# Performance work log

Measured on AMD Instinct MI355X. Metric: run time of the kernel, lower is better.

The kernel has to match this reference:

```python
import jax, jax.numpy as jnp
import numpy as np

B, S, D, H = 2, 2048, 1024, 16
DH = D // H
EPS = 1e-6
MASK_VALUE = -1e30


def layer_norm(x, g, b):
    mu = jnp.mean(x, axis=-1, keepdims=True)
    var = jnp.mean(jnp.square(x - mu), axis=-1, keepdims=True)
    return (x - mu) * jax.lax.rsqrt(var + EPS) * g + b


def setup_inputs() -> dict:
    key = jax.random.key(0)
    ks = jax.random.split(key, 8)
    scale = 1.0 / np.sqrt(D)
    return {
        "x": jax.random.normal(ks[0], (B, S, D), dtype=jnp.float32),
        "mask": jnp.ones((B, S), dtype=jnp.float32),
        "Wq": jax.random.normal(ks[1], (D, D), dtype=jnp.float32) * scale,
        "bq": jnp.zeros((D,), dtype=jnp.float32),
        "Wk": jax.random.normal(ks[2], (D, D), dtype=jnp.float32) * scale,
        "bk": jnp.zeros((D,), dtype=jnp.float32),
        "Wv": jax.random.normal(ks[3], (D, D), dtype=jnp.float32) * scale,
        "bv": jnp.zeros((D,), dtype=jnp.float32),
        "Wo": jax.random.normal(ks[4], (D, D), dtype=jnp.float32) * scale,
        "bo": jnp.zeros((D,), dtype=jnp.float32),
        "g1": jnp.ones((D,), dtype=jnp.float32),
        "b1": jnp.zeros((D,), dtype=jnp.float32),
        "g2": jnp.ones((D,), dtype=jnp.float32),
        "b2": jnp.zeros((D,), dtype=jnp.float32),
    }


def reference(x, mask, Wq, bq, Wk, bk, Wv, bv, Wo, bo, g1, b1, g2, b2):
    # Dropout is identity in eval mode.
    h = layer_norm(x, g1, b1)  # [B,S,D]
    # Conv1D with kernel_size=1 == per-token linear with weight [out,in]
    def proj(W, bias):
        return (jnp.einsum('bsd,ed->bse', h, W) + bias).reshape(B, S, H, DH).transpose(0, 2, 1, 3)
    q = proj(Wq, bq)  # [B,H,S,DH]
    k = proj(Wk, bk)
    v = proj(Wv, bv)
    scores = jnp.einsum('bhqd,bhkd->bhqk', q, k) / np.sqrt(DH)
    scores = scores + (1.0 - mask)[:, None, None, :] * MASK_VALUE
    probs = jax.nn.softmax(scores, axis=-1)
    attn = jnp.einsum('bhqk,bhkd->bhqd', probs, v)  # [B,H,S,DH]
    attn = attn.transpose(0, 2, 1, 3).reshape(B, S, D)
    residual = attn + x
    out = layer_norm(residual, g2, b2)
    out = jnp.einsum('bsd,ed->bse', out, Wo) + bo
    return out + residual
```

## Files before the change

kernel.cpp:

```cpp
#include <hip/hip_runtime.h>
#include <hip/hip_bf16.h>

typedef unsigned short u16;
typedef unsigned int u32;
typedef __attribute__((ext_vector_type(8))) short s16x8;
typedef __attribute__((ext_vector_type(4))) float f32x4;
typedef __attribute__((ext_vector_type(16))) float f32x16;
typedef __attribute__((ext_vector_type(4))) u16 u16x4;

#define SLEN 2048
#define DMODEL 1024
#define NHEAD 16
#define DHEAD 64
#define LDQK 2048
#define VSTRIDE 4096
#define LOG2E 1.4426950408889634f

__device__ __forceinline__ u16 f2bf(float f) {
  union { __hip_bfloat16 h; u16 u; } c;
  c.h = __float2bfloat16(f);
  return c.u;
}

__device__ __forceinline__ u32 pk2(float a, float b) {
  union { __hip_bfloat162 h2; u32 u; } c;
  float2 f2; f2.x = a; f2.y = b;
  c.h2 = __float22bfloat162_rn(f2);
  return c.u;
}

__device__ __forceinline__ void gload_lds16(const u16* gsrc, u16* lds) {
  __builtin_amdgcn_global_load_lds((const __attribute__((address_space(1))) void*)gsrc,
                                   (__attribute__((address_space(3))) void*)lds, 16, 0, 0);
}

__device__ __forceinline__ s16x8 make_pa(int hi, const float* p) {
  u32 A0 = pk2(p[0], p[1]), A1 = pk2(p[2], p[3]);
  u32 A2 = pk2(p[4], p[5]), A3 = pk2(p[6], p[7]);
  u32 S0 = (u32)__shfl_xor((int)A0, 32);
  u32 S1 = (u32)__shfl_xor((int)A1, 32);
  u32 S2 = (u32)__shfl_xor((int)A2, 32);
  u32 S3 = (u32)__shfl_xor((int)A3, 32);
  union { u32 w[4]; s16x8 v; } pw;
  pw.w[0] = hi ? S2 : A0;
  pw.w[1] = hi ? S3 : A1;
  pw.w[2] = hi ? A2 : S0;
  pw.w[3] = hi ? A3 : S1;
  return pw.v;
}

__device__ __forceinline__ void ln_body(
    int row, int t, const float* __restrict__ xa,
    const float* __restrict__ g, const float* __restrict__ bb,
    u16* __restrict__ outb) {
  const size_t base = (size_t)row * DMODEL;
  float4 v = *((const float4*)(xa + base) + t);
  float s1 = v.x + v.y + v.z + v.w;
  float s2 = v.x * v.x + v.y * v.y + v.z * v.z + v.w * v.w;
#pragma unroll
  for (int d = 1; d < 64; d <<= 1) { s1 += __shfl_xor(s1, d); s2 += __shfl_xor(s2, d); }
  __shared__ float red[8];
  if ((t & 63) == 0) { red[(t >> 6) * 2] = s1; red[(t >> 6) * 2 + 1] = s2; }
  __syncthreads();
  s1 = red[0] + red[2] + red[4] + red[6];
  s2 = red[1] + red[3] + red[5] + red[7];
  const float mu = s1 * (1.0f / 1024.0f);
  const float var = s2 * (1.0f / 1024.0f) - mu * mu;
  const float rs = rsqrtf(var + 1e-6f);
  const int c = t * 4;
  float o0 = (v.x - mu) * rs * g[c + 0] + bb[c + 0];
  float o1 = (v.y - mu) * rs * g[c + 1] + bb[c + 1];
  float o2 = (v.z - mu) * rs * g[c + 2] + bb[c + 2];
  float o3 = (v.w - mu) * rs * g[c + 3] + bb[c + 3];
  u16x4 o = { f2bf(o0), f2bf(o1), f2bf(o2), f2bf(o3) };
  *((u16x4*)(outb + base) + t) = o;
}

__global__ __launch_bounds__(256) void prep_kernel(
    const float* __restrict__ x,
    const float* __restrict__ Wq, const float* __restrict__ Wk, const float* __restrict__ Wv,
    const float* __restrict__ Wo, const float* __restrict__ bq, const float* __restrict__ bk,
    const float* __restrict__ bv, const float* __restrict__ mask,
    const float* __restrict__ g1, const float* __restrict__ b1,
    u16* __restrict__ Wqkv, u16* __restrict__ Wob, float* __restrict__ bias_qkv,
    float* __restrict__ am, u32* __restrict__ amflag, u16* __restrict__ h_bf) {
  const int bid = blockIdx.x;
  if (bid >= 4096) {
    ln_body(bid - 4096, threadIdx.x, x, g1, b1, h_bf);
    return;
  }
  const int t = bid * 256 + threadIdx.x;
  float4 v;
  u16* dst;
  if (t < 786432) {
    const int idx = t * 4;
    const int sec = idx >> 20;
    const int off = idx & 1048575;
    const float* src = (sec == 0) ? Wq : (sec == 1) ? Wk : Wv;
    v = *(const float4*)(src + off);
    dst = Wqkv + idx;
  } else {
    const int idx = (t - 786432) * 4;
    v = *(const float4*)(Wo + idx);
    dst = Wob + idx;
  }
  u16x4 o = { f2bf(v.x), f2bf(v.y), f2bf(v.z), f2bf(v.w) };
  *(u16x4*)dst = o;
  if (t < 768) {
    const int idx = t * 4;
    const int sec = idx >> 10;
    const int off = idx & 1023;
    const float* src = (sec == 0) ? bq : (sec == 1) ? bk : bv;
    *(float4*)(bias_qkv + idx) = *(const float4*)(src + off);
  }
  if (t < 1024) {
    const int idx = t * 4;
    float4 mk = *(const float4*)(mask + idx);
    const float C = -1e30f * LOG2E;
    float4 o2 = { (1.f - mk.x) * C, (1.f - mk.y) * C,
                  (1.f - mk.z) * C, (1.f - mk.w) * C };
    *(float4*)(am + idx) = o2;
  }
  if (t < 64) {
    const int bb = t >> 5, tile = t & 31;
    u32 fl = 0;
    for (int j = 0; j < 64; ++j)
      fl |= (mask[bb * SLEN + tile * 64 + j] != 1.0f) ? 1u : 0u;
    amflag[t] = fl;
  }
}

__global__ __launch_bounds__(256) void ln_kernel(
    const float* __restrict__ xa, const float* __restrict__ g,
    const float* __restrict__ bb, u16* __restrict__ outb) {
  ln_body(blockIdx.x, threadIdx.x, xa, g, bb, outb);
}

__device__ __forceinline__ void gemm_core(
    const u16* __restrict__ A, const u16* __restrict__ B,
    const float* __restrict__ bias, const float* __restrict__ res,
    u16* __restrict__ outb, float* __restrict__ outf,
    int M, int N, int K, int m0, int n0, int mode,
    u16* As, u16* Bs) {
  const int t = threadIdx.x;
  const int l = t & 63, w = t >> 6, lr = l & 15, lg = l >> 4;
  const int wm = w >> 1, wn = w & 1;

  const f32x4 z4 = {0.f, 0.f, 0.f, 0.f};
  f32x4 acc[4][4];
#pragma unroll
  for (int i = 0; i < 4; ++i)
#pragma unroll
    for (int j = 0; j < 4; ++j) acc[i][j] = z4;

  for (int kt = 0; kt < K; kt += 64) {
#pragma unroll
    for (int p = 0; p < 4; ++p) {
      const int idx = p * 256 + t;
      const int row = idx >> 3;
      const int blk = idx & 7;
      const int sb = blk ^ (row & 7);
      gload_lds16(A + (size_t)(m0 + row) * K + kt + sb * 8, &As[idx * 8]);
      gload_lds16(B + (size_t)(n0 + row) * K + kt + sb * 8, &Bs[idx * 8]);
    }
    asm volatile("s_waitcnt vmcnt(0)" ::: "memory");
    __syncthreads();

#pragma unroll
    for (int ks = 0; ks < 2; ++ks) {
      s16x8 af[4], bfr[4];
#pragma unroll
      for (int mi = 0; mi < 4; ++mi) {
        const int row = wm * 64 + mi * 16 + lr;
        af[mi] = *(const s16x8*)&As[row * 64 + (((ks * 4 + lg) ^ (row & 7)) & 7) * 8];
      }
#pragma unroll
      for (int ni = 0; ni < 4; ++ni) {
        const int row = wn * 64 + ni * 16 + lr;
        bfr[ni] = *(const s16x8*)&Bs[row * 64 + (((ks * 4 + lg) ^ (row & 7)) & 7) * 8];
      }
#pragma unroll
      for (int mi = 0; mi < 4; ++mi)
#pragma unroll
        for (int ni = 0; ni < 4; ++ni)
          acc[mi][ni] = __builtin_amdgcn_mfma_f32_16x16x32_bf16(af[mi], bfr[ni], acc[mi][ni], 0, 0, 0);
    }
    __syncthreads();
  }

#pragma unroll
  for (int mi = 0; mi < 4; ++mi)
#pragma unroll
    for (int ni = 0; ni < 4; ++ni) {
      const int col = n0 + wn * 64 + ni * 16 + lr;
#pragma unroll
      for (int r = 0; r < 4; ++r) {
        const int rowb = m0 + wm * 64 + mi * 16 + lg * 4 + r;
        float vv = acc[mi][ni][r];
        if (mode == 2) {
          vv += bias[rowb];
          outb[(size_t)rowb * N + col] = f2bf(vv);
        } else if (mode == 0) {
          vv += bias[col];
          if (col < 1024) vv *= 0.125f * LOG2E;
          outb[(size_t)rowb * N + col] = f2bf(vv);
        } else {
          vv += bias[col] + res[(size_t)rowb * N + col];
          outf[(size_t)rowb * N + col] = vv;
        }
      }
    }
}

__global__ __launch_bounds__(256) void qkv_gemm_kernel(
    const u16* __restrict__ h_bf, const u16* __restrict__ Wqkv,
    const float* __restrict__ biasq, u16* __restrict__ qkbuf, u16* __restrict__ vT) {
  __shared__ __align__(16) u16 As[128 * 64];
  __shared__ __align__(16) u16 Bs[128 * 64];
  const int bid = blockIdx.x;
  const int lid = (bid & 7) * 96 + (bid >> 3);
  if (lid < 512) {
    gemm_core(h_bf, Wqkv, biasq, nullptr, qkbuf, nullptr,
              4096, 2048, 1024, (lid & 31) * 128, (lid >> 5) * 128, 0, As, Bs);
  } else {
    const int id = lid - 512;
    gemm_core(Wqkv + (size_t)2048 * 1024, h_bf, biasq + 2048, nullptr, vT, nullptr,
              1024, 4096, 1024, (id & 7) * 128, (id >> 3) * 128, 2, As, Bs);
  }
}

__global__ __launch_bounds__(256) void out_gemm_kernel(
    const u16* __restrict__ h2, const u16* __restrict__ Wob,
    const float* __restrict__ bo, const float* __restrict__ res,
    float* __restrict__ outf) {
  __shared__ __align__(16) u16 As[128 * 64];
  __shared__ __align__(16) u16 Bs[128 * 64];
  const int bid = blockIdx.x;
  const int lid = (bid & 7) * 32 + (bid >> 3);
  gemm_core(h2, Wob, bo, res, nullptr, outf,
            4096, 1024, 1024, (lid & 31) * 128, (lid >> 5) * 128, 1, As, Bs);
}

__global__ __launch_bounds__(256) void attn_kernel(
    const u16* __restrict__ qk, const u16* __restrict__ vt,
    const float* __restrict__ am, const u32* __restrict__ amflag,
    const float* __restrict__ x, float* __restrict__ out) {
  const int did = blockIdx.x;
  const int lid = (did & 7) * 64 + (did >> 3);
  const int qb = lid & 15;
  const int h = (lid >> 4) & 15;
  const int b = lid >> 8;

  const int t = threadIdx.x;
  const int l = t & 63, w = t >> 6;
  const int l31 = l & 31;
  const int hi = l >> 5;
  const int hi4 = hi * 4;
  const int sw = l31 & 7;

  __shared__ __align__(16) u16 Ks[2][64 * 64];
  __shared__ __align__(16) u16 Vs[2][64 * 64];
  __shared__ u32 amFlagS[32];
  __shared__ float bcastS[4][32];

  const int q0 = qb * 128 + w * 32;

  const u16* qrow = qk + (size_t)(b * SLEN + q0 + l31) * LDQK + h * DHEAD + hi * 8;
  s16x8 qf[4];
#pragma unroll
  for (int f = 0; f < 4; ++f) qf[f] = *(const s16x8*)(qrow + f * 16);

  if (t < 32) amFlagS[t] = amflag[b * 32 + t];

  const u16* kbase = qk + (size_t)(b * SLEN) * LDQK + DMODEL + h * DHEAD;
  const u16* vtbase = vt + (size_t)(h * DHEAD) * VSTRIDE + b * SLEN;

#define STAGE(kt, buf)                                                              \
  {                                                                                 \
    _Pragma("unroll")                                                               \
    for (int p = 0; p < 2; ++p) {                                                   \
      const int idx = p * 256 + t;                                                  \
      const int row = idx >> 3;                                                     \
      const int blk = idx & 7;                                                      \
      const int sb = blk ^ (row & 7);                                               \
      gload_lds16(kbase + (size_t)((kt) * 64 + row) * LDQK + sb * 8,                \
                  &Ks[buf][idx * 8]);                                               \
    }                                                                               \
    _Pragma("unroll")                                                               \
    for (int p = 0; p < 2; ++p) {                                                   \
      const int idx = p * 256 + t;                                                  \
      const int dh = idx >> 3;                                                      \
      const int blk = idx & 7;                                                      \
      const int sb = blk ^ (dh & 7);                                                \
      gload_lds16(vtbase + (size_t)dh * VSTRIDE + (kt) * 64 + sb * 8,               \
                  &Vs[buf][idx * 8]);                                               \
    }                                                                               \
  }

  f32x16 oA, oB;
#pragma unroll
  for (int r = 0; r < 16; ++r) { oA[r] = 0.f; oB[r] = 0.f; }
  float lsum = 0.f;

  STAGE(0, 0);
  asm volatile("s_waitcnt vmcnt(0)" ::: "memory");
  __syncthreads();

  int cur = 0;
  for (int kt = 0; kt < SLEN / 64; ++kt) {
    if (kt + 1 < SLEN / 64) STAGE(kt + 1, cur ^ 1);

    f32x16 sA, sB;
#pragma unroll
    for (int r = 0; r < 16; ++r) { sA[r] = 0.f; sB[r] = 0.f; }
    __builtin_amdgcn_s_setprio(1);
#pragma unroll
    for (int f = 0; f < 4; ++f) {
      const int c = 2 * f + hi;
      s16x8 kA = *(const s16x8*)&Ks[cur][l31 * 64 + ((c ^ sw) & 7) * 8];
      s16x8 kB = *(const s16x8*)&Ks[cur][(32 + l31) * 64 + ((c ^ sw) & 7) * 8];
      sA = __builtin_amdgcn_mfma_f32_32x32x16_bf16(kA, qf[f], sA, 0, 0, 0);
      sB = __builtin_amdgcn_mfma_f32_32x32x16_bf16(kB, qf[f], sB, 0, 0, 0);
    }
    __builtin_amdgcn_s_setprio(0);

    const int kv0 = kt * 64;
    if (amFlagS[kt]) {
#pragma unroll
      for (int r = 0; r < 16; ++r) {
        const int rid = (r & 3) + ((r >> 2) << 3) + hi4;
        sA[r] += am[b * SLEN + kv0 + rid];
        sB[r] += am[b * SLEN + kv0 + 32 + rid];
      }
    }

    float pA_[16], pB_[16];
#pragma unroll
    for (int r = 0; r < 16; ++r) {
      pA_[r] = __builtin_amdgcn_exp2f(sA[r]);
      pB_[r] = __builtin_amdgcn_exp2f(sB[r]);
    }
    float s8[8];
#pragma unroll
    for (int i = 0; i < 8; ++i)
      s8[i] = (pA_[2 * i] + pA_[2 * i + 1]) + (pB_[2 * i] + pB_[2 * i + 1]);
#pragma unroll
    for (int i = 0; i < 4; ++i) s8[i] += s8[i + 4];
    s8[0] += s8[2]; s8[1] += s8[3];
    lsum += s8[0] + s8[1];

    s16x8 pa0 = make_pa(hi, pA_);
    s16x8 pa1 = make_pa(hi, pA_ + 8);
    s16x8 pa2 = make_pa(hi, pB_);
    s16x8 pa3 = make_pa(hi, pB_ + 8);

    __builtin_amdgcn_s_setprio(1);
#pragma unroll
    for (int s = 0; s < 4; ++s) {
      const int c = 2 * s + hi;
      s16x8 vA = *(const s16x8*)&Vs[cur][l31 * 64 + ((c ^ sw) & 7) * 8];
      s16x8 vB = *(const s16x8*)&Vs[cur][(32 + l31) * 64 + ((c ^ sw) & 7) * 8];
      const s16x8 pas = (s == 0) ? pa0 : (s == 1) ? pa1 : (s == 2) ? pa2 : pa3;
      oA = __builtin_amdgcn_mfma_f32_32x32x16_bf16(pas, vA, oA, 0, 0, 0);
      oB = __builtin_amdgcn_mfma_f32_32x32x16_bf16(pas, vB, oB, 0, 0, 0);
    }
    __builtin_amdgcn_s_setprio(0);

    asm volatile("s_waitcnt vmcnt(0)" ::: "memory");
    __syncthreads();
    cur ^= 1;
  }

  lsum += __shfl_xor(lsum, 32);
  bcastS[w][l31] = 1.0f / lsum;
  const size_t rowoff = (size_t)(b * SLEN + q0) * DMODEL + h * DHEAD + l31;
  float* outp = out + rowoff;
  const float* xp = x + rowoff;
#pragma unroll
  for (int r = 0; r < 16; ++r) {
    const int rid = (r & 3) + ((r >> 2) << 3) + hi4;
    const float rv = bcastS[w][rid];
    outp[(size_t)rid * DMODEL] = oA[r] * rv + xp[(size_t)rid * DMODEL];
    outp[(size_t)rid * DMODEL + 32] = oB[r] * rv + xp[(size_t)rid * DMODEL + 32];
  }
#undef STAGE
}

extern "C" void kernel_launch(void* const* d_in, const int* in_sizes, int n_in,
                              void* d_out, int out_size, void* d_ws, size_t ws_size,
                              hipStream_t stream) {
  const float* x    = (const float*)d_in[0];
  const float* mask = (const float*)d_in[1];
  const float* Wq   = (const float*)d_in[2];
  const float* bq   = (const float*)d_in[3];
  const float* Wk   = (const float*)d_in[4];
  const float* bk   = (const float*)d_in[5];
  const float* Wv   = (const float*)d_in[6];
  const float* bv   = (const float*)d_in[7];
  const float* Wo   = (const float*)d_in[8];
  const float* bo   = (const float*)d_in[9];
  const float* g1   = (const float*)d_in[10];
  const float* b1   = (const float*)d_in[11];
  const float* g2   = (const float*)d_in[12];
  const float* b2   = (const float*)d_in[13];
  float* out = (float*)d_out;
  char* ws = (char*)d_ws;

  u16*   h_bf  = (u16*)(ws + 0);
  u16*   Wqkv  = (u16*)(ws + ((size_t)8 << 20));
  u16*   Wob   = (u16*)(ws + ((size_t)14 << 20));
  float* biasq = (float*)(ws + ((size_t)16 << 20));
  float* amv   = (float*)(ws + ((size_t)16 << 20) + (64 << 10));
  u32*   amfl  = (u32*)(ws + ((size_t)16 << 20) + (128 << 10));
  u16*   qkbuf = (u16*)(ws + ((size_t)17 << 20));
  u16*   vT2   = (u16*)(ws + ((size_t)33 << 20));
  float* resb  = (float*)(ws + ((size_t)41 << 20));
  u16*   h2_bf = (u16*)(ws + 0);

  prep_kernel<<<8192, 256, 0, stream>>>(x, Wq, Wk, Wv, Wo, bq, bk, bv, mask, g1, b1,
                                        Wqkv, Wob, biasq, amv, amfl, h_bf);
  qkv_gemm_kernel<<<768, 256, 0, stream>>>(h_bf, Wqkv, biasq, qkbuf, vT2);
  attn_kernel<<<512, 256, 0, stream>>>(qkbuf, vT2, amv, amfl, x, resb);
  ln_kernel<<<4096, 256, 0, stream>>>(resb, g2, b2, h2_bf);
  out_gemm_kernel<<<256, 256, 0, stream>>>(h2_bf, Wob, bo, resb, out);
}
```

Baseline: 146.2 us.

## Pipeline GEMM K-loop with four-stage LDS ring and use permlane32 swap in attention

The shared GEMM core moves from a single-buffered 64-wide K tile with a full wait and two barriers per step to a four-buffer ring of 32-wide K tiles. Three tiles are prefetched ahead, with partial vmcnt waits and one barrier per step, so global-to-LDS loads overlap MFMA work. In attention, the P-fragment repack replaces four cross-half shuffles and selects with two v_permlane32_swap instructions. LDS per GEMM block doubles to 64 KB, which may reduce occupancy.

```diff
diff --git a/kernel.cpp b/kernel.cpp
--- a/kernel.cpp
+++ b/kernel.cpp
@@ -34,18 +34,13 @@
                                    (__attribute__((address_space(3))) void*)lds, 16, 0, 0);
 }
 
-__device__ __forceinline__ s16x8 make_pa(int hi, const float* p) {
+__device__ __forceinline__ s16x8 make_pa(const float* p) {
   u32 A0 = pk2(p[0], p[1]), A1 = pk2(p[2], p[3]);
   u32 A2 = pk2(p[4], p[5]), A3 = pk2(p[6], p[7]);
-  u32 S0 = (u32)__shfl_xor((int)A0, 32);
-  u32 S1 = (u32)__shfl_xor((int)A1, 32);
-  u32 S2 = (u32)__shfl_xor((int)A2, 32);
-  u32 S3 = (u32)__shfl_xor((int)A3, 32);
+  asm("v_permlane32_swap_b32 %0, %1" : "+v"(A0), "+v"(A2));
+  asm("v_permlane32_swap_b32 %0, %1" : "+v"(A1), "+v"(A3));
   union { u32 w[4]; s16x8 v; } pw;
-  pw.w[0] = hi ? S2 : A0;
-  pw.w[1] = hi ? S3 : A1;
-  pw.w[2] = hi ? A2 : S0;
-  pw.w[3] = hi ? A3 : S1;
+  pw.w[0] = A0; pw.w[1] = A1; pw.w[2] = A2; pw.w[3] = A3;
   return pw.v;
 }
 
@@ -153,39 +148,61 @@
 #pragma unroll
     for (int j = 0; j < 4; ++j) acc[i][j] = z4;
 
-  for (int kt = 0; kt < K; kt += 64) {
-#pragma unroll
-    for (int p = 0; p < 4; ++p) {
-      const int idx = p * 256 + t;
-      const int row = idx >> 3;
-      const int blk = idx & 7;
-      const int sb = blk ^ (row & 7);
-      gload_lds16(A + (size_t)(m0 + row) * K + kt + sb * 8, &As[idx * 8]);
-      gload_lds16(B + (size_t)(n0 + row) * K + kt + sb * 8, &Bs[idx * 8]);
-    }
-    asm volatile("s_waitcnt vmcnt(0)" ::: "memory");
-    __syncthreads();
-
-#pragma unroll
-    for (int ks = 0; ks < 2; ++ks) {
-      s16x8 af[4], bfr[4];
-#pragma unroll
-      for (int mi = 0; mi < 4; ++mi) {
-        const int row = wm * 64 + mi * 16 + lr;
-        af[mi] = *(const s16x8*)&As[row * 64 + (((ks * 4 + lg) ^ (row & 7)) & 7) * 8];
-      }
-#pragma unroll
-      for (int ni = 0; ni < 4; ++ni) {
-        const int row = wn * 64 + ni * 16 + lr;
-        bfr[ni] = *(const s16x8*)&Bs[row * 64 + (((ks * 4 + lg) ^ (row & 7)) & 7) * 8];
-      }
-#pragma unroll
-      for (int mi = 0; mi < 4; ++mi)
-#pragma unroll
-        for (int ni = 0; ni < 4; ++ni)
-          acc[mi][ni] = __builtin_amdgcn_mfma_f32_16x16x32_bf16(af[mi], bfr[ni], acc[mi][ni], 0, 0, 0);
-    }
-    __syncthreads();
+  const int nt = K >> 5;
+
+#define GSTAGE(tt, buf)                                                         \
+  {                                                                             \
+    _Pragma("unroll")                                                           \
+    for (int p = 0; p < 2; ++p) {                                               \
+      const int c = p * 256 + t;                                                \
+      const int row = c >> 2, blk = c & 3;                                      \
+      const int sb = blk ^ (row & 3);                                           \
+      gload_lds16(A + (size_t)(m0 + row) * K + (tt) * 32 + sb * 8,              \
+                  &As[(buf) * 4096 + c * 8]);                                   \
+    }                                                                           \
+    _Pragma("unroll")                                                           \
+    for (int p = 0; p < 2; ++p) {                                               \
+      const int c = p * 256 + t;                                                \
+      const int row = c >> 2, blk = c & 3;                                      \
+      const int sb = blk ^ (row & 3);                                           \
+      gload_lds16(B + (size_t)(n0 + row) * K + (tt) * 32 + sb * 8,              \
+                  &Bs[(buf) * 4096 + c * 8]);                                   \
+    }                                                                           \
+  }
+
+  GSTAGE(0, 0);
+  GSTAGE(1, 1);
+  GSTAGE(2, 2);
+  asm volatile("s_waitcnt vmcnt(8)" ::: "memory");
+  __builtin_amdgcn_s_barrier();
+
+  for (int tt = 0; tt < nt; ++tt) {
+    const int buf = tt & 3;
+    if (tt + 3 < nt) GSTAGE(tt + 3, (tt + 3) & 3);
+
+    s16x8 af[4], bfr[4];
+#pragma unroll
+    for (int mi = 0; mi < 4; ++mi) {
+      const int row = wm * 64 + mi * 16 + lr;
+      af[mi] = *(const s16x8*)&As[buf * 4096 + row * 32 + ((lg ^ (row & 3)) & 3) * 8];
+    }
+#pragma unroll
+    for (int ni = 0; ni < 4; ++ni) {
+      const int row = wn * 64 + ni * 16 + lr;
+      bfr[ni] = *(const s16x8*)&Bs[buf * 4096 + row * 32 + ((lg ^ (row & 3)) & 3) * 8];
+    }
+    __builtin_amdgcn_s_setprio(1);
+#pragma unroll
+    for (int mi = 0; mi < 4; ++mi)
+#pragma unroll
+      for (int ni = 0; ni < 4; ++ni)
+        acc[mi][ni] = __builtin_amdgcn_mfma_f32_16x16x32_bf16(af[mi], bfr[ni], acc[mi][ni], 0, 0, 0);
+    __builtin_amdgcn_s_setprio(0);
+
+    if (tt + 3 < nt)      asm volatile("s_waitcnt vmcnt(8)" ::: "memory");
+    else if (tt + 2 < nt) asm volatile("s_waitcnt vmcnt(4)" ::: "memory");
+    else if (tt + 1 < nt) asm volatile("s_waitcnt vmcnt(0)" ::: "memory");
+    __builtin_amdgcn_s_barrier();
   }
 
 #pragma unroll
@@ -210,13 +227,14 @@
         }
       }
     }
+#undef GSTAGE
 }
 
 __global__ __launch_bounds__(256) void qkv_gemm_kernel(
     const u16* __restrict__ h_bf, const u16* __restrict__ Wqkv,
     const float* __restrict__ biasq, u16* __restrict__ qkbuf, u16* __restrict__ vT) {
-  __shared__ __align__(16) u16 As[128 * 64];
-  __shared__ __align__(16) u16 Bs[128 * 64];
+  __shared__ __align__(16) u16 As[4 * 4096];
+  __shared__ __align__(16) u16 Bs[4 * 4096];
   const int bid = blockIdx.x;
   const int lid = (bid & 7) * 96 + (bid >> 3);
   if (lid < 512) {
@@ -233,8 +251,8 @@
     const u16* __restrict__ h2, const u16* __restrict__ Wob,
     const float* __restrict__ bo, const float* __restrict__ res,
     float* __restrict__ outf) {
-  __shared__ __align__(16) u16 As[128 * 64];
-  __shared__ __align__(16) u16 Bs[128 * 64];
+  __shared__ __align__(16) u16 As[4 * 4096];
+  __shared__ __align__(16) u16 Bs[4 * 4096];
   const int bid = blockIdx.x;
   const int lid = (bid & 7) * 32 + (bid >> 3);
   gemm_core(h2, Wob, bo, res, nullptr, outf,
@@ -349,10 +367,10 @@
     s8[0] += s8[2]; s8[1] += s8[3];
     lsum += s8[0] + s8[1];
 
-    s16x8 pa0 = make_pa(hi, pA_);
-    s16x8 pa1 = make_pa(hi, pA_ + 8);
-    s16x8 pa2 = make_pa(hi, pB_);
-    s16x8 pa3 = make_pa(hi, pB_ + 8);
+    s16x8 pa0 = make_pa(pA_);
+    s16x8 pa1 = make_pa(pA_ + 8);
+    s16x8 pa2 = make_pa(pB_);
+    s16x8 pa3 = make_pa(pB_ + 8);
 
     __builtin_amdgcn_s_setprio(1);
 #pragma unroll
```

Measured after the change: 154.5 us. 5.7% more time.
